# Kernel optimization log

Measured on AMD Instinct MI355X. Metric: run time of the kernel, lower is better.

Reference implementation:

```python
import jax, jax.numpy as jnp
import numpy as np

B, C, H, W = 2, 512, 64, 64
G = 32          # GroupNorm groups
EPS = 1e-6


def setup_inputs() -> dict:
    key = jax.random.key(0)
    ks = jax.random.split(key, 10)
    s = 1.0 / np.sqrt(C)
    return {
        "x": jax.random.normal(ks[0], (B, C, H, W), dtype=jnp.float32),
        "gn_w": jnp.ones((C,), jnp.float32),
        "gn_b": jnp.zeros((C,), jnp.float32),
        "wq": jax.random.normal(ks[1], (C, C), jnp.float32) * s,
        "bq": jnp.zeros((C,), jnp.float32),
        "wk": jax.random.normal(ks[2], (C, C), jnp.float32) * s,
        "bk": jnp.zeros((C,), jnp.float32),
        "wv": jax.random.normal(ks[3], (C, C), jnp.float32) * s,
        "bv": jnp.zeros((C,), jnp.float32),
        "wo": jax.random.normal(ks[4], (C, C), jnp.float32) * s,
        "bo": jnp.zeros((C,), jnp.float32),
    }


def reference(x, gn_w, gn_b, wq, bq, wk, bk, wv, bv, wo, bo):
    b, c, h, w = x.shape
    n = h * w
    # GroupNorm(32, eps=1e-6, affine)
    xg = x.reshape(b, G, c // G, h, w)
    mu = xg.mean(axis=(2, 3, 4), keepdims=True)
    var = ((xg - mu) ** 2).mean(axis=(2, 3, 4), keepdims=True)
    hn = ((xg - mu) * jax.lax.rsqrt(var + EPS)).reshape(b, c, h, w)
    hn = hn * gn_w[None, :, None, None] + gn_b[None, :, None, None]
    # 1x1 convs == per-pixel linear over channels; tokens: b n c
    hf = hn.reshape(b, c, n)
    q = jnp.einsum('oc,bcn->bno', wq, hf) + bq  # [b, n, c]
    k = jnp.einsum('oc,bcn->bno', wk, hf) + bk
    v = jnp.einsum('oc,bcn->bno', wv, hf) + bv
    scale = jnp.asarray(c, x.dtype) ** -0.5
    att = jax.nn.softmax(jnp.einsum('bic,bjc->bij', q, k) * scale, axis=-1)
    o = jnp.einsum('bij,bjc->bic', att, v)      # [b, n, c]
    out = jnp.einsum('oc,bnc->bno', wo, o) + bo # proj_out
    return x + out.transpose(0, 2, 1).reshape(b, c, h, w)
```

## Files before the change

### kernel.cpp

```cpp
#include <hip/hip_runtime.h>
#include <hip/hip_bf16.h>


typedef float f32x4 __attribute__((ext_vector_type(4)));
typedef __bf16 bf16x8 __attribute__((ext_vector_type(8)));

typedef const __attribute__((address_space(1))) unsigned char* gas_p;
typedef __attribute__((address_space(3))) unsigned char* las_p;

__device__ __forceinline__ void gload_lds16(const void* g, void* l) {
  __builtin_amdgcn_global_load_lds((gas_p)g, (las_p)l, 16, 0, 0);
}

__global__ __launch_bounds__(256) void prelude_k(
    const float* __restrict__ wq, const float* __restrict__ wk,
    const float* __restrict__ wv, const float* __restrict__ wo,
    __hip_bfloat16* __restrict__ wqkb, __hip_bfloat16* __restrict__ wvb,
    __hip_bfloat16* __restrict__ wob, const float* __restrict__ bq,
    const float* __restrict__ bk, float* __restrict__ bqk,
    const float* __restrict__ x, float* __restrict__ stats) {
  int bid = blockIdx.x;
  if (bid < 4096) {
    const float* src;
    __hip_bfloat16* dst;
    if (bid < 1024)      { src = wq; dst = wqkb; }
    else if (bid < 2048) { src = wk; dst = wqkb + 262144; }
    else if (bid < 3072) { src = wv; dst = wvb; }
    else                 { src = wo; dst = wob; }
    int i = (bid & 1023) * 256 + threadIdx.x;
    dst[i] = __float2bfloat16(src[i]);
    return;
  }
  if (bid < 4160) {
    int bg = bid - 4096;
    const float4* p = (const float4*)(x + (size_t)bg * 65536);
    float s = 0.f, s2 = 0.f;
    for (int i = threadIdx.x; i < 16384; i += 256) {
      float4 v = p[i];
      s  += v.x + v.y + v.z + v.w;
      s2 += v.x * v.x + v.y * v.y + v.z * v.z + v.w * v.w;
    }
#pragma unroll
    for (int off = 32; off > 0; off >>= 1) {
      s  += __shfl_xor(s, off);
      s2 += __shfl_xor(s2, off);
    }
    __shared__ float rs[4], rs2[4];
    int wid = threadIdx.x >> 6, lane = threadIdx.x & 63;
    if (lane == 0) { rs[wid] = s; rs2[wid] = s2; }
    __syncthreads();
    if (threadIdx.x == 0) {
      float S  = rs[0] + rs[1] + rs[2] + rs[3];
      float S2 = rs2[0] + rs2[1] + rs2[2] + rs2[3];
      float mean = S * (1.f / 65536.f);
      float var  = S2 * (1.f / 65536.f) - mean * mean;
      stats[bg * 2]     = mean;
      stats[bg * 2 + 1] = rsqrtf(var + 1e-6f);
    }
    return;
  }
  for (int j = threadIdx.x; j < 1024; j += 256)
    bqk[j] = (j < 512) ? bq[j] : bk[j - 512];
}

__global__ __launch_bounds__(256) void gn_apply_k(const float* __restrict__ x,
                                                  const float* __restrict__ stats,
                                                  const float* __restrict__ gw,
                                                  const float* __restrict__ gb,
                                                  __hip_bfloat16* __restrict__ hf) {
  int c0 = blockIdx.x * 64, n0 = blockIdx.y * 64, b = blockIdx.z;
  __shared__ float tile[64][65];
  int tid = threadIdx.x;
  int cl = tid >> 2, q = tid & 3;
  int c = c0 + cl;
  float mean = stats[(b * 32 + (c >> 4)) * 2];
  float rstd = stats[(b * 32 + (c >> 4)) * 2 + 1];
  float sc = rstd * gw[c];
  float sh = gb[c] - mean * sc;
  const float* xr = x + ((size_t)(b * 512 + c0 + cl)) * 4096 + n0 + q * 16;
#pragma unroll
  for (int j = 0; j < 4; j++) {
    float4 v = *(const float4*)(xr + 4 * j);
    int n = q * 16 + 4 * j;
    tile[cl][n]     = v.x * sc + sh;
    tile[cl][n + 1] = v.y * sc + sh;
    tile[cl][n + 2] = v.z * sc + sh;
    tile[cl][n + 3] = v.w * sc + sh;
  }
  __syncthreads();
  int nl = tid >> 2, ch = q * 16;
  bf16x8 o0, o1;
#pragma unroll
  for (int l = 0; l < 8; l++) {
    o0[l] = (__bf16)tile[ch + l][nl];
    o1[l] = (__bf16)tile[ch + 8 + l][nl];
  }
  __hip_bfloat16* op = hf + ((size_t)(b * 4096 + n0 + nl)) * 512 + c0 + ch;
  *(uint4*)op = *(uint4*)&o0;
  *(uint4*)(op + 8) = *(uint4*)&o1;
}

__global__ __launch_bounds__(256, 4) void qkv_k(
    const __hip_bfloat16* __restrict__ hf, const __hip_bfloat16* __restrict__ wqk,
    const __hip_bfloat16* __restrict__ wv, const float* __restrict__ bqk,
    const float* __restrict__ bv, __hip_bfloat16* __restrict__ qk,
    __hip_bfloat16* __restrict__ vT) {
  bool isV = blockIdx.x >= 8;
  int m0 = isV ? (blockIdx.x - 8) * 128 : blockIdx.y * 128;
  int n0 = isV ? blockIdx.y * 128 : blockIdx.x * 128;
  const __hip_bfloat16* A  = isV ? wv : hf;
  const __hip_bfloat16* Bm = isV ? hf : wqk;

  __shared__ __align__(16) unsigned char smem[34816];
  __hip_bfloat16* As  = (__hip_bfloat16*)smem;
  __hip_bfloat16* Bs  = As + 8192;
  __hip_bfloat16* epi = (__hip_bfloat16*)smem;

  int tid  = threadIdx.x;
  int wvx  = tid >> 6, lane = tid & 63;
  int wr   = (wvx >> 1) * 64, wc = (wvx & 1) * 64;
  int quad = lane >> 4, l16 = lane & 15;

  int srow = wvx * 32 + (lane >> 2);
  int scol = (lane & 3) * 8;
  const __hip_bfloat16* gA0 = A  + (size_t)(m0 + srow) * 512 + scol;
  const __hip_bfloat16* gA1 = gA0 + (size_t)16 * 512;
  const __hip_bfloat16* gB0 = Bm + (size_t)(n0 + srow) * 512 + scol;
  const __hip_bfloat16* gB1 = gB0 + (size_t)16 * 512;

  auto stage = [&](int kk, int bsel) {
    int lb = bsel * 4096 + wvx * 1024;
    gload_lds16(gA0 + kk, &As[lb]);
    gload_lds16(gA1 + kk, &As[lb + 512]);
    gload_lds16(gB0 + kk, &Bs[lb]);
    gload_lds16(gB1 + kk, &Bs[lb + 512]);
  };

  f32x4 acc[4][4] = {};
  stage(0, 0);
  for (int kt = 0; kt < 16; kt++) {
    __syncthreads();
    if (kt + 1 < 16) stage((kt + 1) << 5, (kt + 1) & 1);
    const __hip_bfloat16* Ab = &As[(kt & 1) * 4096];
    const __hip_bfloat16* Bb = &Bs[(kt & 1) * 4096];
    bf16x8 af[4], bfr[4];
#pragma unroll
    for (int i = 0; i < 4; i++)
      af[i] = *(const bf16x8*)&Ab[(wr + i * 16 + l16) * 32 + quad * 8];
#pragma unroll
    for (int j = 0; j < 4; j++)
      bfr[j] = *(const bf16x8*)&Bb[(wc + j * 16 + l16) * 32 + quad * 8];
#pragma unroll
    for (int i = 0; i < 4; i++)
#pragma unroll
      for (int j = 0; j < 4; j++)
        acc[i][j] = __builtin_amdgcn_mfma_f32_16x16x32_bf16(af[i], bfr[j],
                                                            acc[i][j], 0, 0, 0);
  }

  float bj[4], bm[4][4];
  if (!isV) {
#pragma unroll
    for (int j = 0; j < 4; j++) bj[j] = bqk[n0 + wc + j * 16 + l16];
  } else {
#pragma unroll
    for (int i = 0; i < 4; i++)
#pragma unroll
      for (int r = 0; r < 4; r++)
        bm[i][r] = bv[m0 + wr + i * 16 + quad * 4 + r];
  }
  __syncthreads();
#pragma unroll
  for (int i = 0; i < 4; i++)
#pragma unroll
    for (int j = 0; j < 4; j++)
#pragma unroll
      for (int r = 0; r < 4; r++) {
        int ml = wr + i * 16 + quad * 4 + r;
        int nl = wc + j * 16 + l16;
        float v = acc[i][j][r] + (isV ? bm[i][r] : bj[j]);
        epi[ml * 136 + nl] = __float2bfloat16(v);
      }
  __syncthreads();
  int mr = tid >> 1, h = tid & 1;
  const __hip_bfloat16* rowp = &epi[mr * 136 + h * 64];
  if (!isV) {
    __hip_bfloat16* o = qk + (size_t)(m0 + mr) * 1024 + n0 + h * 64;
#pragma unroll
    for (int c = 0; c < 8; c++)
      *(uint4*)(o + c * 8) = *(const uint4*)(rowp + c * 8);
  } else {
    int b = (n0 + h * 64) >> 12, t = (n0 + h * 64) & 4095;
    __hip_bfloat16* o = vT + ((size_t)(b * 512 + m0 + mr)) * 4096 + t;
#pragma unroll
    for (int c = 0; c < 8; c++)
      *(uint4*)(o + c * 8) = *(const uint4*)(rowp + c * 8);
  }
}

__global__ __launch_bounds__(512, 2) void attn_k(
    const __hip_bfloat16* __restrict__ qk, const __hip_bfloat16* __restrict__ vT,
    __hip_bfloat16* __restrict__ part, float* __restrict__ rsum) {
  const float scale = 0.044194173824159216f;
  int bid = blockIdx.x;
  int g2 = bid & 7;
  int b = g2 >> 2, spl = (g2 >> 1) & 1;
  int qtile = (g2 & 1) * 32 + (bid >> 3);

  const __hip_bfloat16* qkb = qk + (size_t)b * 4194304;
  const __hip_bfloat16* vTb = vT + (size_t)b * 2097152;

  __shared__ __align__(16) unsigned char smem[133120];
  __hip_bfloat16* Qs = (__hip_bfloat16*)smem;
  __hip_bfloat16* Ks = (__hip_bfloat16*)(smem + 16384);
  __hip_bfloat16* Vs = (__hip_bfloat16*)(smem + 49152);
  __hip_bfloat16* Ps = (__hip_bfloat16*)(smem + 114688);
  float* Rs = (float*)(smem + 132096);

  int tid = threadIdx.x, wv = tid >> 6, lane = tid & 63;
  int quad = lane >> 4, l16 = lane & 15;
  int q0 = (wv >> 2) * 32;
  int kvc0 = (wv & 3) * 32;
  int wd0 = (wv & 3) * 128;

  int srow8 = lane >> 3;
  int schk = ((lane & 7) ^ srow8) * 8;
  const __hip_bfloat16* gQ = qkb + (size_t)(qtile * 64 + wv * 8 + srow8) * 1024 + schk;
  const __hip_bfloat16* gK0 =
      qkb + (size_t)(spl * 2048 + wv * 16 + srow8) * 1024 + 512 + schk;
  const __hip_bfloat16* gK1 = gK0 + (size_t)8 * 1024;
  const __hip_bfloat16* gV = vTb + (size_t)(wv * 64 + (lane >> 2)) * 4096 +
                             spl * 2048 + (lane & 3) * 8;

  auto stageQK = [&](int t, int s, int bsel) {
    int koff = t * 131072 + s * 64;
    gload_lds16(gQ + s * 64, &Qs[bsel * 4096 + wv * 512]);
    gload_lds16(gK0 + koff, &Ks[bsel * 8192 + wv * 1024]);
    gload_lds16(gK1 + koff, &Ks[bsel * 8192 + wv * 1024 + 512]);
  };
  auto stageV = [&](int t, int sub, int vb) {
    const __hip_bfloat16* g = gV + t * 128 + sub * 32;
#pragma unroll
    for (int c = 0; c < 4; c++)
      gload_lds16(g + (size_t)(c * 16) * 4096, &Vs[vb * 16384 + wv * 2048 + c * 512]);
  };

  f32x4 accS[2][2] = {};
  f32x4 accO[8][2] = {};
  float rsr[8] = {};

  stageQK(0, 0, 0);
  for (int t = 0; t < 16; t++) {
    for (int s = 0; s < 8; s++) {
      __syncthreads();
      if (s < 7) stageQK(t, s + 1, (s + 1) & 1);
      else stageV(t, 0, 0);
      const __hip_bfloat16* Qb = &Qs[(s & 1) * 4096];
      const __hip_bfloat16* Kb = &Ks[(s & 1) * 8192];
      bf16x8 aq[2][2], bkf[2][2];
#pragma unroll
      for (int ii = 0; ii < 2; ii++)
#pragma unroll
        for (int kk = 0; kk < 2; kk++) {
          int r = q0 + ii * 16 + l16;
          aq[ii][kk] = *(const bf16x8*)&Qb[r * 64 + ((kk * 4 + quad) ^ (r & 7)) * 8];
        }
#pragma unroll
      for (int jj = 0; jj < 2; jj++)
#pragma unroll
        for (int kk = 0; kk < 2; kk++) {
          int r = kvc0 + jj * 16 + l16;
          bkf[jj][kk] = *(const bf16x8*)&Kb[r * 64 + ((kk * 4 + quad) ^ (r & 7)) * 8];
        }
#pragma unroll
      for (int ii = 0; ii < 2; ii++)
#pragma unroll
        for (int jj = 0; jj < 2; jj++)
#pragma unroll
          for (int kk = 0; kk < 2; kk++)
            accS[ii][jj] = __builtin_amdgcn_mfma_f32_16x16x32_bf16(
                aq[ii][kk], bkf[jj][kk], accS[ii][jj], 0, 0, 0);
    }
#pragma unroll
    for (int ii = 0; ii < 2; ii++)
#pragma unroll
      for (int jj = 0; jj < 2; jj++) {
#pragma unroll
        for (int rr = 0; rr < 4; rr++) {
          float p = __expf(accS[ii][jj][rr] * scale);
          rsr[ii * 4 + rr] += p;
          Ps[(q0 + ii * 16 + quad * 4 + rr) * 136 + kvc0 + jj * 16 + l16] =
              __float2bfloat16(p);
        }
        accS[ii][jj] = (f32x4){0.f, 0.f, 0.f, 0.f};
      }
    for (int sub = 0; sub < 4; sub++) {
      __syncthreads();
      if (sub < 3) stageV(t, sub + 1, (sub + 1) & 1);
      else if (t + 1 < 16) stageQK(t + 1, 0, 0);
      const __hip_bfloat16* Vb = &Vs[(sub & 1) * 16384];
      bf16x8 pa[2], bvf[8];
#pragma unroll
      for (int ii = 0; ii < 2; ii++) {
        int r = q0 + ii * 16 + l16;
        pa[ii] = *(const bf16x8*)&Ps[r * 136 + sub * 32 + quad * 8];
      }
#pragma unroll
      for (int jj = 0; jj < 8; jj++) {
        int r = wd0 + jj * 16 + l16;
        bvf[jj] = *(const bf16x8*)&Vb[r * 32 + quad * 8];
      }
#pragma unroll
      for (int jj = 0; jj < 8; jj++)
#pragma unroll
        for (int ii = 0; ii < 2; ii++)
          accO[jj][ii] = __builtin_amdgcn_mfma_f32_16x16x32_bf16(
              pa[ii], bvf[jj], accO[jj][ii], 0, 0, 0);
    }
  }

  size_t pbase = ((size_t)(spl * 2 + b) * 4096 + qtile * 64) * 512;
#pragma unroll
  for (int ii = 0; ii < 2; ii++)
#pragma unroll
    for (int rr = 0; rr < 4; rr++) {
      int row = q0 + ii * 16 + quad * 4 + rr;
#pragma unroll
      for (int jj = 0; jj < 8; jj++)
        part[pbase + (size_t)row * 512 + wd0 + jj * 16 + l16] =
            __float2bfloat16(accO[jj][ii][rr]);
    }
#pragma unroll
  for (int k = 0; k < 8; k++)
#pragma unroll
    for (int off = 1; off < 16; off <<= 1) rsr[k] += __shfl_xor(rsr[k], off);
  if (l16 == 0) {
#pragma unroll
    for (int ii = 0; ii < 2; ii++)
#pragma unroll
      for (int rr = 0; rr < 4; rr++)
        Rs[(wv & 3) * 64 + q0 + ii * 16 + quad * 4 + rr] = rsr[ii * 4 + rr];
  }
  __syncthreads();
  if (tid < 64)
    rsum[spl * 8192 + b * 4096 + qtile * 64 + tid] =
        Rs[tid] + Rs[64 + tid] + Rs[128 + tid] + Rs[192 + tid];
}

__global__ __launch_bounds__(256) void reduce2_k(
    const __hip_bfloat16* __restrict__ part, const float* __restrict__ rsum,
    __hip_bfloat16* __restrict__ obuf) {
  size_t i8 = (size_t)blockIdx.x * 256 + threadIdx.x;
  size_t perb = 262144;
  size_t b = i8 / perb, r = i8 - b * perb;
  int t = (int)(r >> 6);
  float ps = rsum[b * 4096 + t] + rsum[8192 + b * 4096 + t];
  float inv = 1.f / ps;
  bf16x8 v0 = ((const bf16x8*)part)[b * perb + r];
  bf16x8 v1 = ((const bf16x8*)part)[(2 + b) * perb + r];
  bf16x8 o;
#pragma unroll
  for (int l = 0; l < 8; l++)
    o[l] = (__bf16)(((float)v0[l] + (float)v1[l]) * inv);
  ((bf16x8*)obuf)[b * perb + r] = o;
}

__global__ __launch_bounds__(256, 2) void oproj_k(
    const __hip_bfloat16* __restrict__ Wo, const __hip_bfloat16* __restrict__ O,
    float* __restrict__ out, const float* __restrict__ bias,
    const float* __restrict__ resid) {
  int m0 = blockIdx.y * 64, n0 = blockIdx.x * 128, bb = blockIdx.z;
  O += (size_t)bb * 4096 * 512;
  size_t cbase = (size_t)bb * 512 * 4096;

  __shared__ __align__(16) unsigned char smem[24576];
  __hip_bfloat16* As  = (__hip_bfloat16*)smem;
  __hip_bfloat16* Bs  = As + 4096;
  __hip_bfloat16* epi = (__hip_bfloat16*)smem;

  int tid = threadIdx.x, wv = tid >> 6, lane = tid & 63;
  int wr = (wv >> 1) * 32, wc = (wv & 1) * 64;
  int quad = lane >> 4, l16 = lane & 15;

  int lr = lane >> 2, scol = (lane & 3) * 8;
  const __hip_bfloat16* gA  = Wo + (size_t)(m0 + wv * 16 + lr) * 512 + scol;
  const __hip_bfloat16* gB0 = O  + (size_t)(n0 + wv * 32 + lr) * 512 + scol;
  const __hip_bfloat16* gB1 = gB0 + (size_t)16 * 512;

  auto stage = [&](int kk, int bsel) {
    gload_lds16(gA + kk, &As[bsel * 2048 + wv * 512]);
    gload_lds16(gB0 + kk, &Bs[bsel * 4096 + wv * 1024]);
    gload_lds16(gB1 + kk, &Bs[bsel * 4096 + wv * 1024 + 512]);
  };

  f32x4 acc[2][4] = {};
  stage(0, 0);
  for (int kt = 0; kt < 16; kt++) {
    __syncthreads();
    if (kt + 1 < 16) stage((kt + 1) << 5, (kt + 1) & 1);
    const __hip_bfloat16* Ab = &As[(kt & 1) * 2048];
    const __hip_bfloat16* Bb = &Bs[(kt & 1) * 4096];
    bf16x8 af[2], bfr[4];
#pragma unroll
    for (int i = 0; i < 2; i++)
      af[i] = *(const bf16x8*)&Ab[(wr + i * 16 + l16) * 32 + quad * 8];
#pragma unroll
    for (int j = 0; j < 4; j++)
      bfr[j] = *(const bf16x8*)&Bb[(wc + j * 16 + l16) * 32 + quad * 8];
#pragma unroll
    for (int i = 0; i < 2; i++)
#pragma unroll
      for (int j = 0; j < 4; j++)
        acc[i][j] = __builtin_amdgcn_mfma_f32_16x16x32_bf16(af[i], bfr[j],
                                                            acc[i][j], 0, 0, 0);
  }

  float pre[2][4];
#pragma unroll
  for (int i = 0; i < 2; i++)
#pragma unroll
    for (int r = 0; r < 4; r++)
      pre[i][r] = bias[m0 + wr + i * 16 + quad * 4 + r];
  __syncthreads();
#pragma unroll
  for (int i = 0; i < 2; i++)
#pragma unroll
    for (int j = 0; j < 4; j++)
#pragma unroll
      for (int r = 0; r < 4; r++)
        epi[(wr + i * 16 + quad * 4 + r) * 136 + wc + j * 16 + l16] =
            __float2bfloat16(acc[i][j][r] + pre[i][r]);
  __syncthreads();
  int mr = tid >> 2, seg = tid & 3;
  const __hip_bfloat16* rowp = &epi[mr * 136 + seg * 32];
  size_t obase = cbase + (size_t)(m0 + mr) * 4096 + n0 + seg * 32;
#pragma unroll
  for (int c = 0; c < 4; c++) {
    bf16x8 val = *(const bf16x8*)(rowp + c * 8);
    size_t idx = obase + c * 8;
    float4 r0 = *(const float4*)&resid[idx];
    float4 r1 = *(const float4*)&resid[idx + 4];
    float4 o0, o1;
    o0.x = r0.x + (float)val[0]; o0.y = r0.y + (float)val[1];
    o0.z = r0.z + (float)val[2]; o0.w = r0.w + (float)val[3];
    o1.x = r1.x + (float)val[4]; o1.y = r1.y + (float)val[5];
    o1.z = r1.z + (float)val[6]; o1.w = r1.w + (float)val[7];
    *(float4*)&out[idx] = o0;
    *(float4*)&out[idx + 4] = o1;
  }
}

extern "C" void kernel_launch(void* const* d_in, const int* in_sizes, int n_in,
                              void* d_out, int out_size, void* d_ws,
                              size_t ws_size, hipStream_t stream) {
  const float* xp  = (const float*)d_in[0];
  const float* gwp = (const float*)d_in[1];
  const float* gbp = (const float*)d_in[2];
  const float* wqp = (const float*)d_in[3];
  const float* bqp = (const float*)d_in[4];
  const float* wkp = (const float*)d_in[5];
  const float* bkp = (const float*)d_in[6];
  const float* wvp = (const float*)d_in[7];
  const float* bvp = (const float*)d_in[8];
  const float* wop = (const float*)d_in[9];
  const float* bop = (const float*)d_in[10];
  float* outp = (float*)d_out;

  char* w = (char*)d_ws;
  size_t off = 0;
  auto alloc = [&](size_t bytes) {
    void* p = w + off;
    off += (bytes + 255) & ~(size_t)255;
    return p;
  };
  float* stats         = (float*)alloc(64 * 2 * sizeof(float));
  __hip_bfloat16* hf   = (__hip_bfloat16*)alloc((size_t)2 * 4096 * 512 * 2);
  __hip_bfloat16* wqkb = (__hip_bfloat16*)alloc((size_t)1024 * 512 * 2);
  __hip_bfloat16* wvb  = (__hip_bfloat16*)alloc((size_t)512 * 512 * 2);
  __hip_bfloat16* wob  = (__hip_bfloat16*)alloc((size_t)512 * 512 * 2);
  float* bqk           = (float*)alloc(1024 * sizeof(float));
  float* rsum          = (float*)alloc((size_t)2 * 2 * 4096 * sizeof(float));
  __hip_bfloat16* qk   = (__hip_bfloat16*)alloc((size_t)2 * 4096 * 1024 * 2);
  __hip_bfloat16* vT   = (__hip_bfloat16*)alloc((size_t)2 * 512 * 4096 * 2);
  __hip_bfloat16* obuf = (__hip_bfloat16*)alloc((size_t)2 * 4096 * 512 * 2);
  __hip_bfloat16* part = (__hip_bfloat16*)alloc((size_t)4 * 4096 * 512 * 2);

  prelude_k<<<4161, 256, 0, stream>>>(wqp, wkp, wvp, wop, wqkb, wvb, wob,
                                      bqp, bkp, bqk, xp, stats);

  gn_apply_k<<<dim3(8, 64, 2), 256, 0, stream>>>(xp, stats, gwp, gbp, hf);

  qkv_k<<<dim3(12, 64, 1), 256, 0, stream>>>(hf, wqkb, wvb, bqk, bvp, qk, vT);

  attn_k<<<256, 512, 0, stream>>>(qk, vT, part, rsum);

  reduce2_k<<<2048, 256, 0, stream>>>(part, rsum, obuf);

  oproj_k<<<dim3(32, 8, 2), 256, 0, stream>>>(wob, obuf, outp, bop, xp);
}
```

Before: 282.8 us.

## Split attention KV four ways and read V fragments directly from global

The attention kernel now splits the key/value range four ways instead of two and launches twice as many blocks. V is no longer staged through shared memory; each wave loads its V MFMA fragments straight from global memory into registers. This frees the V buffer and roughly halves the shared-memory footprint, so two blocks can fit per CU and occupancy should rise. The trade-offs are uncoalesced global V loads that lean on cache, a doubled partial-output buffer, and a reduce kernel that must now sum four partials and four row sums.

```diff
diff --git a/kernel.cpp b/kernel.cpp
--- a/kernel.cpp
+++ b/kernel.cpp
@@ -203,19 +203,18 @@
     __hip_bfloat16* __restrict__ part, float* __restrict__ rsum) {
   const float scale = 0.044194173824159216f;
   int bid = blockIdx.x;
-  int g2 = bid & 7;
-  int b = g2 >> 2, spl = (g2 >> 1) & 1;
-  int qtile = (g2 & 1) * 32 + (bid >> 3);
+  int g = bid & 7;
+  int b = g >> 2, spl = g & 3;
+  int qtile = bid >> 3;
 
   const __hip_bfloat16* qkb = qk + (size_t)b * 4194304;
   const __hip_bfloat16* vTb = vT + (size_t)b * 2097152;
 
-  __shared__ __align__(16) unsigned char smem[133120];
+  __shared__ __align__(16) unsigned char smem[67584];
   __hip_bfloat16* Qs = (__hip_bfloat16*)smem;
   __hip_bfloat16* Ks = (__hip_bfloat16*)(smem + 16384);
-  __hip_bfloat16* Vs = (__hip_bfloat16*)(smem + 49152);
-  __hip_bfloat16* Ps = (__hip_bfloat16*)(smem + 114688);
-  float* Rs = (float*)(smem + 132096);
+  __hip_bfloat16* Ps = (__hip_bfloat16*)(smem + 49152);
+  float* Rs = (float*)(smem + 66560);
 
   int tid = threadIdx.x, wv = tid >> 6, lane = tid & 63;
   int quad = lane >> 4, l16 = lane & 15;
@@ -225,12 +224,11 @@
 
   int srow8 = lane >> 3;
   int schk = ((lane & 7) ^ srow8) * 8;
-  const __hip_bfloat16* gQ = qkb + (size_t)(qtile * 64 + wv * 8 + srow8) * 1024 + schk;
+  const __hip_bfloat16* gQ =
+      qkb + (size_t)(qtile * 64 + wv * 8 + srow8) * 1024 + schk;
   const __hip_bfloat16* gK0 =
-      qkb + (size_t)(spl * 2048 + wv * 16 + srow8) * 1024 + 512 + schk;
+      qkb + (size_t)(spl * 1024 + wv * 16 + srow8) * 1024 + 512 + schk;
   const __hip_bfloat16* gK1 = gK0 + (size_t)8 * 1024;
-  const __hip_bfloat16* gV = vTb + (size_t)(wv * 64 + (lane >> 2)) * 4096 +
-                             spl * 2048 + (lane & 3) * 8;
 
   auto stageQK = [&](int t, int s, int bsel) {
     int koff = t * 131072 + s * 64;
@@ -238,23 +236,19 @@
     gload_lds16(gK0 + koff, &Ks[bsel * 8192 + wv * 1024]);
     gload_lds16(gK1 + koff, &Ks[bsel * 8192 + wv * 1024 + 512]);
   };
-  auto stageV = [&](int t, int sub, int vb) {
-    const __hip_bfloat16* g = gV + t * 128 + sub * 32;
-#pragma unroll
-    for (int c = 0; c < 4; c++)
-      gload_lds16(g + (size_t)(c * 16) * 4096, &Vs[vb * 16384 + wv * 2048 + c * 512]);
-  };
+
+  const __hip_bfloat16* vbase =
+      vTb + (size_t)(wd0 + l16) * 4096 + spl * 1024 + quad * 8;
 
   f32x4 accS[2][2] = {};
   f32x4 accO[8][2] = {};
   float rsr[8] = {};
 
   stageQK(0, 0, 0);
-  for (int t = 0; t < 16; t++) {
+  for (int t = 0; t < 8; t++) {
     for (int s = 0; s < 8; s++) {
       __syncthreads();
       if (s < 7) stageQK(t, s + 1, (s + 1) & 1);
-      else stageV(t, 0, 0);
       const __hip_bfloat16* Qb = &Qs[(s & 1) * 4096];
       const __hip_bfloat16* Kb = &Ks[(s & 1) * 8192];
       bf16x8 aq[2][2], bkf[2][2];
@@ -294,22 +288,18 @@
         }
         accS[ii][jj] = (f32x4){0.f, 0.f, 0.f, 0.f};
       }
+    __syncthreads();
+    if (t + 1 < 8) stageQK(t + 1, 0, 0);
     for (int sub = 0; sub < 4; sub++) {
-      __syncthreads();
-      if (sub < 3) stageV(t, sub + 1, (sub + 1) & 1);
-      else if (t + 1 < 16) stageQK(t + 1, 0, 0);
-      const __hip_bfloat16* Vb = &Vs[(sub & 1) * 16384];
-      bf16x8 pa[2], bvf[8];
-#pragma unroll
-      for (int ii = 0; ii < 2; ii++) {
-        int r = q0 + ii * 16 + l16;
-        pa[ii] = *(const bf16x8*)&Ps[r * 136 + sub * 32 + quad * 8];
-      }
-#pragma unroll
-      for (int jj = 0; jj < 8; jj++) {
-        int r = wd0 + jj * 16 + l16;
-        bvf[jj] = *(const bf16x8*)&Vb[r * 32 + quad * 8];
-      }
+      bf16x8 bvf[8];
+      const __hip_bfloat16* vp = vbase + t * 128 + sub * 32;
+#pragma unroll
+      for (int jj = 0; jj < 8; jj++)
+        bvf[jj] = *(const bf16x8*)(vp + jj * 65536);
+      bf16x8 pa[2];
+#pragma unroll
+      for (int ii = 0; ii < 2; ii++)
+        pa[ii] = *(const bf16x8*)&Ps[(q0 + ii * 16 + l16) * 136 + sub * 32 + quad * 8];
 #pragma unroll
       for (int jj = 0; jj < 8; jj++)
 #pragma unroll
@@ -317,6 +307,7 @@
           accO[jj][ii] = __builtin_amdgcn_mfma_f32_16x16x32_bf16(
               pa[ii], bvf[jj], accO[jj][ii], 0, 0, 0);
     }
+    __syncthreads();
   }
 
   size_t pbase = ((size_t)(spl * 2 + b) * 4096 + qtile * 64) * 512;
@@ -354,14 +345,19 @@
   size_t perb = 262144;
   size_t b = i8 / perb, r = i8 - b * perb;
   int t = (int)(r >> 6);
-  float ps = rsum[b * 4096 + t] + rsum[8192 + b * 4096 + t];
+  float ps = rsum[b * 4096 + t] + rsum[8192 + b * 4096 + t] +
+             rsum[16384 + b * 4096 + t] + rsum[24576 + b * 4096 + t];
   float inv = 1.f / ps;
-  bf16x8 v0 = ((const bf16x8*)part)[b * perb + r];
-  bf16x8 v1 = ((const bf16x8*)part)[(2 + b) * perb + r];
+  float acc[8] = {};
+#pragma unroll
+  for (int sp = 0; sp < 4; sp++) {
+    bf16x8 v = ((const bf16x8*)part)[(sp * 2 + b) * perb + r];
+#pragma unroll
+    for (int l = 0; l < 8; l++) acc[l] += (float)v[l];
+  }
   bf16x8 o;
 #pragma unroll
-  for (int l = 0; l < 8; l++)
-    o[l] = (__bf16)(((float)v0[l] + (float)v1[l]) * inv);
+  for (int l = 0; l < 8; l++) o[l] = (__bf16)(acc[l] * inv);
   ((bf16x8*)obuf)[b * perb + r] = o;
 }
 
@@ -479,11 +475,11 @@
   __hip_bfloat16* wvb  = (__hip_bfloat16*)alloc((size_t)512 * 512 * 2);
   __hip_bfloat16* wob  = (__hip_bfloat16*)alloc((size_t)512 * 512 * 2);
   float* bqk           = (float*)alloc(1024 * sizeof(float));
-  float* rsum          = (float*)alloc((size_t)2 * 2 * 4096 * sizeof(float));
+  float* rsum          = (float*)alloc((size_t)4 * 2 * 4096 * sizeof(float));
   __hip_bfloat16* qk   = (__hip_bfloat16*)alloc((size_t)2 * 4096 * 1024 * 2);
   __hip_bfloat16* vT   = (__hip_bfloat16*)alloc((size_t)2 * 512 * 4096 * 2);
   __hip_bfloat16* obuf = (__hip_bfloat16*)alloc((size_t)2 * 4096 * 512 * 2);
-  __hip_bfloat16* part = (__hip_bfloat16*)alloc((size_t)4 * 4096 * 512 * 2);
+  __hip_bfloat16* part = (__hip_bfloat16*)alloc((size_t)8 * 4096 * 512 * 2);
 
   prelude_k<<<4161, 256, 0, stream>>>(wqp, wkp, wvp, wop, wqkb, wvb, wob,
                                       bqp, bkp, bqk, xp, stats);
@@ -492,7 +488,7 @@
 
   qkv_k<<<dim3(12, 64, 1), 256, 0, stream>>>(hf, wqkb, wvb, bqk, bvp, qk, vT);
 
-  attn_k<<<256, 512, 0, stream>>>(qk, vT, part, rsum);
+  attn_k<<<512, 512, 0, stream>>>(qk, vT, part, rsum);
 
   reduce2_k<<<2048, 256, 0, stream>>>(part, rsum, obuf);
 
```

Result: slower. 377.8 us (+33.6%).
